# Kernel tuning notes

Hardware: AMD Instinct MI355X
Metric: run time of the kernel (lower is better)

Reference implementation:

```python
import jax, jax.numpy as jnp
import numpy as np

B, T, D = 8, 2048, 1024   # batch, seq_len (== block_size), n_embed
HS = 128                   # head_size

def setup_inputs() -> dict:
    key = jax.random.key(0)
    kx, kk, kq, kv = jax.random.split(key, 4)
    s = D ** -0.5  # torch Linear default init scale ~ U(-1/sqrt(in), 1/sqrt(in))
    x  = jax.random.normal(kx, (B, T, D), dtype=jnp.float32)
    Wk = jax.random.uniform(kk, (HS, D), jnp.float32, -s, s)
    Wq = jax.random.uniform(kq, (HS, D), jnp.float32, -s, s)
    Wv = jax.random.uniform(kv, (HS, D), jnp.float32, -s, s)
    return {"x": x, "Wk": Wk, "Wq": Wq, "Wv": Wv}

def reference(x, Wk, Wq, Wv):
    # single-head causal self-attention; dropout disabled (eval mode)
    Tlen = x.shape[1]
    k = jnp.einsum('btd,hd->bth', x, Wk)   # [B,T,HS]
    q = jnp.einsum('btd,hd->bth', x, Wq)
    v = jnp.einsum('btd,hd->bth', x, Wv)
    scale = Wk.shape[0] ** -0.5
    scores = jnp.einsum('bth,bsh->bts', q, k) * scale   # [B,T,T]
    causal = jnp.tril(jnp.ones((Tlen, Tlen), dtype=bool))
    scores = jnp.where(causal, scores, -jnp.inf)
    weights = jax.nn.softmax(scores, axis=-1)
    out = jnp.einsum('bts,bsh->bth', weights, v)        # [B,T,HS]
    return out
```

## Files before the change

### kernel.cpp

```cpp
#include <hip/hip_runtime.h>
#include <hip/hip_bf16.h>
#include <math.h>

#define BATCH_N 8
#define SEQ_T   2048
#define DIM_D   1024
#define HS_N    128

using bf16x8_t = __attribute__((ext_vector_type(8))) __bf16;
using bf16x4_t = __attribute__((ext_vector_type(4))) __bf16;
using f32x4_t  = __attribute__((ext_vector_type(4))) float;

__device__ __forceinline__ f32x4_t mfma_16x16x32(bf16x8_t a, bf16x8_t b, f32x4_t c) {
  return __builtin_amdgcn_mfma_f32_16x16x32_bf16(a, b, c, 0, 0, 0);
}

__device__ __forceinline__ void async_cp16(const void* g, void* l) {
  __builtin_amdgcn_global_load_lds(
      (const __attribute__((address_space(1))) unsigned int*)g,
      (__attribute__((address_space(3))) unsigned int*)l, 16, 0, 0);
}

#define BAR()      __builtin_amdgcn_s_barrier()
#define FENCE()    asm volatile("" ::: "memory")
#define WAIT_VM(n) asm volatile("s_waitcnt vmcnt(" #n ")" ::: "memory")
#define WAIT_LGKM0 asm volatile("s_waitcnt lgkmcnt(0)" ::: "memory")

__global__ __launch_bounds__(256) void castw_kernel(
    const float* __restrict__ Wk, const float* __restrict__ Wq,
    const float* __restrict__ Wv, __bf16* __restrict__ Wb,
    unsigned int* __restrict__ km) {
  if (blockIdx.x == 0 && threadIdx.x < 8) km[threadIdx.x] = 0u;
  int idx = blockIdx.x * 256 + threadIdx.x;
  int e   = idx * 4;
  int row = e >> 10;
  int col = e & 1023;
  const float* src;
  float sc = 1.0f;
  if (row < 128) {
    src = Wk + row * DIM_D + col;
  } else if (row < 256) {
    src = Wq + (row - 128) * DIM_D + col;
    sc  = 0.08838834764831845f;
  } else {
    src = Wv + (row - 256) * DIM_D + col;
  }
  float4 v = *(const float4*)src;
  bf16x4_t o;
  o[0] = (__bf16)(v.x * sc); o[1] = (__bf16)(v.y * sc);
  o[2] = (__bf16)(v.z * sc); o[3] = (__bf16)(v.w * sc);
  *(bf16x4_t*)(Wb + e) = o;
}

__global__ __launch_bounds__(256, 2) void proj_kernel(
    const float* __restrict__ x, const __bf16* __restrict__ Wb,
    __bf16* __restrict__ Qb, __bf16* __restrict__ Kb, __bf16* __restrict__ Vt,
    unsigned int* __restrict__ km) {
  __shared__ __align__(16) char psmem[57344];

  const int tid  = threadIdx.x;
  const int lane = tid & 63;
  const int wave = tid >> 6;
  const int lr = lane & 15;
  const int lq = lane >> 4;
  const int m0 = blockIdx.x * 32;

  f32x4_t acc[2][6];
  #pragma unroll
  for (int mt = 0; mt < 2; ++mt)
    #pragma unroll
    for (int nt = 0; nt < 6; ++nt) acc[mt][nt] = (f32x4_t){0.f, 0.f, 0.f, 0.f};

  auto stageA = [&](int kt) {
    char* As = psmem + (kt & 1) * 4096;
    const int row = wave * 8 + (lane >> 3);
    const int u16 = lane & 7;
    const int su16 = (((u16 >> 1) ^ (row & 3)) << 1) | (u16 & 1);
    async_cp16(x + (size_t)(m0 + row) * DIM_D + kt * 32 + su16 * 4,
               As + wave * 1024);
  };

  auto stageB = [&](int kt) {
    __bf16* Bs = (__bf16*)(psmem + 8192 + (kt & 1) * 24576);
    for (int c = wave; c < 24; c += 4) {
      const int row = c * 16 + (lane >> 2);
      const int u   = (lane & 3) ^ ((row >> 1) & 3);
      async_cp16(Wb + (size_t)row * DIM_D + kt * 32 + u * 8, Bs + c * 512);
    }
  };

  stageA(0);
  stageB(0);
  __syncthreads();

  for (int kt = 0; kt < 32; ++kt) {
    if (kt + 1 < 32) {
      stageA(kt + 1);
      stageB(kt + 1);
      WAIT_VM(7);
    } else {
      WAIT_VM(0);
    }
    BAR();
    FENCE();

    const float*  As = (const float*)(psmem + (kt & 1) * 4096);
    const __bf16* Bs = (const __bf16*)(psmem + 8192 + (kt & 1) * 24576);

    bf16x8_t af[2];
    #pragma unroll
    for (int mt = 0; mt < 2; ++mt) {
      const int ml   = mt * 16 + lr;
      const int u32r = lq ^ (ml & 3);
      f32x4_t lo = *(const f32x4_t*)(As + ml * 32 + u32r * 8);
      f32x4_t hi = *(const f32x4_t*)(As + ml * 32 + u32r * 8 + 4);
      bf16x8_t a;
      a[0] = (__bf16)lo[0]; a[1] = (__bf16)lo[1];
      a[2] = (__bf16)lo[2]; a[3] = (__bf16)lo[3];
      a[4] = (__bf16)hi[0]; a[5] = (__bf16)hi[1];
      a[6] = (__bf16)hi[2]; a[7] = (__bf16)hi[3];
      af[mt] = a;
    }
    bf16x8_t bfv[6];
    #pragma unroll
    for (int nt = 0; nt < 6; ++nt) {
      const int nl = wave * 96 + nt * 16 + lr;
      bfv[nt] = *(const bf16x8_t*)(&Bs[nl * 32 + ((lq ^ ((nl >> 1) & 3)) * 8)]);
    }
    #pragma unroll
    for (int mt = 0; mt < 2; ++mt)
      #pragma unroll
      for (int nt = 0; nt < 6; ++nt)
        acc[mt][nt] = mfma_16x16x32(af[mt], bfv[nt], acc[mt][nt]);
    WAIT_LGKM0;
    BAR();
    FENCE();
  }

  __syncthreads();
  float* rowss = (float*)psmem;
  if (tid < 32) rowss[tid] = 0.f;
  __syncthreads();
  if (wave < 2) {
    #pragma unroll
    for (int mt = 0; mt < 2; ++mt)
      #pragma unroll
      for (int r = 0; r < 4; ++r) {
        float s = 0.f;
        #pragma unroll
        for (int nt = 0; nt < 6; ++nt)
          if (wave == 0 || nt < 2) s += acc[mt][nt][r] * acc[mt][nt][r];
        s += __shfl_xor(s, 1); s += __shfl_xor(s, 2);
        s += __shfl_xor(s, 4); s += __shfl_xor(s, 8);
        if (lr == 0) atomicAdd(&rowss[mt * 16 + lq * 4 + r], s);
      }
  }
  __syncthreads();
  if (tid < 32) {
    float v = rowss[tid];
    #pragma unroll
    for (int off = 1; off < 32; off <<= 1) v = fmaxf(v, __shfl_xor(v, off));
    if (tid == 0) atomicMax(km + (m0 >> 11), __float_as_uint(v));
  }

  #pragma unroll
  for (int mt = 0; mt < 2; ++mt) {
    const int t0 = m0 + mt * 16 + lq * 4;
    #pragma unroll
    for (int nt = 0; nt < 6; ++nt) {
      const int nn = wave * 96 + nt * 16 + lr;
      if (nn < 256) {
        __bf16* dst = (nn < 128) ? (Kb + nn) : (Qb + (nn - 128));
        #pragma unroll
        for (int r = 0; r < 4; ++r)
          dst[(size_t)(t0 + r) * HS_N] = (__bf16)acc[mt][nt][r];
      } else {
        const int bb = t0 >> 11;
        const int tl = t0 & 2047;
        bf16x4_t o;
        #pragma unroll
        for (int r = 0; r < 4; ++r) o[r] = (__bf16)acc[mt][nt][r];
        *(bf16x4_t*)(Vt + (size_t)bb * (HS_N * SEQ_T) + (size_t)(nn - 256) * SEQ_T + tl) = o;
      }
    }
  }
}

__global__ __launch_bounds__(256, 2) void attn_kernel(
    const __bf16* __restrict__ Qb, const __bf16* __restrict__ Kb,
    const __bf16* __restrict__ Vt, const unsigned int* __restrict__ km,
    __bf16* __restrict__ Opart, float* __restrict__ lpart) {
  __shared__ __align__(16) char smem[81920];
  __bf16* KsBase = (__bf16*)smem;
  __bf16* VsBase = (__bf16*)(smem + 32768);
  float*  Ofl    = (float*)smem;

  const int lane = threadIdx.x & 63;
  const int wave = threadIdx.x >> 6;
  const int lr = lane & 15;
  const int lq = lane >> 4;
  const int bid  = blockIdx.x;
  const int b    = bid & 7;
  const int rest = bid >> 3;
  const int jg   = 15 - (rest >> 2);
  const int p4   = rest & 3;
  const int Q0   = jg * 128;
  const int qa   = Q0 + wave * 32;
  const int ch   = 2 * (jg + 1);
  const int c0   = (p4 * ch) >> 2;
  const int c1   = ((p4 + 1) * ch) >> 2;

  const __bf16* Qbb = Qb + (size_t)b * (SEQ_T * HS_N);
  const __bf16* Kbb = Kb + (size_t)b * (SEQ_T * HS_N);
  const __bf16* Vbb = Vt + (size_t)b * (HS_N * SEQ_T);
  __bf16* pbA = (__bf16*)(smem + 65536 + wave * 4096);
  __bf16* pbB = (__bf16*)(smem + 65536 + wave * 4096 + 2048);

  bf16x8_t qf[2][4];
  #pragma unroll
  for (int t = 0; t < 2; ++t)
    #pragma unroll
    for (int ks = 0; ks < 4; ++ks)
      qf[t][ks] = *(const bf16x8_t*)(Qbb + (size_t)(qa + t * 16 + lr) * HS_N
                                     + ks * 32 + lq * 8);

  const float km2 = __uint_as_float(km[b]);
  float mrow[2][4];
  #pragma unroll
  for (int t = 0; t < 2; ++t) {
    float qn2 = 0.f;
    #pragma unroll
    for (int ks = 0; ks < 4; ++ks)
      #pragma unroll
      for (int j = 0; j < 8; ++j) { float f = (float)qf[t][ks][j]; qn2 += f * f; }
    qn2 += __shfl_xor(qn2, 16);
    qn2 += __shfl_xor(qn2, 32);
    #pragma unroll
    for (int r2 = 0; r2 < 4; ++r2)
      mrow[t][r2] = sqrtf(__shfl(qn2, lq * 4 + r2) * km2);
  }

  f32x4_t Oa[2][8];
  #pragma unroll
  for (int t = 0; t < 2; ++t)
    #pragma unroll
    for (int o = 0; o < 8; ++o) Oa[t][o] = (f32x4_t){0.f, 0.f, 0.f, 0.f};
  float lsum[2][4] = {{0.f,0.f,0.f,0.f},{0.f,0.f,0.f,0.f}};

  auto stage = [&](int bufi, int c) {
    const int kk = c * 64;
    __bf16* Ks = KsBase + bufi * 8192;
    for (int idx = wave; idx < 32; idx += 4) {
      if (idx < 16) {
        const int row = idx * 4 + (lane >> 4);
        const int u   = (lane & 15) ^ (row & 15);
        async_cp16(Kbb + (size_t)(kk + row) * HS_N + u * 8, Ks + idx * 512);
      } else {
        const int i2  = idx - 16;
        const int row = i2 * 8 + (lane >> 3);
        const int u   = (lane & 7) ^ (row & 7);
        async_cp16(Vbb + (size_t)row * SEQ_T + kk + u * 8, VsBase + bufi * 8192 + i2 * 512);
      }
    }
  };

  if (c0 < c1) stage(0, c0);
  __syncthreads();

  for (int c = c0; c < c1; ++c) {
    const int cur = (c - c0) & 1;
    if (c + 1 < c1) {
      stage(cur ^ 1, c + 1);
      WAIT_VM(8);
    } else {
      WAIT_VM(0);
    }
    BAR();
    FENCE();

    const int kk = c * 64;
    const __bf16* Ks = KsBase + cur * 8192;
    const __bf16* Vs = VsBase + cur * 8192;

    f32x4_t s0[4], s1[4];
    #pragma unroll
    for (int nt = 0; nt < 4; ++nt) {
      s0[nt] = (f32x4_t){0.f, 0.f, 0.f, 0.f};
      s1[nt] = (f32x4_t){0.f, 0.f, 0.f, 0.f};
    }
    #pragma unroll
    for (int ks = 0; ks < 4; ++ks)
      #pragma unroll
      for (int nt = 0; nt < 4; ++nt) {
        bf16x8_t kf = *(const bf16x8_t*)(
            &Ks[(nt * 16 + lr) * 128 + (((ks * 4 + lq) ^ lr) * 8)]);
        s0[nt] = mfma_16x16x32(qf[0][ks], kf, s0[nt]);
        s1[nt] = mfma_16x16x32(qf[1][ks], kf, s1[nt]);
      }
    const int q0a = qa, q0b = qa + 16;
    if (kk + 63 > q0a) {
      #pragma unroll
      for (int nt = 0; nt < 4; ++nt) {
        const int col = kk + nt * 16 + lr;
        #pragma unroll
        for (int r2 = 0; r2 < 4; ++r2)
          if (col > q0a + lq * 4 + r2) s0[nt][r2] = -INFINITY;
      }
    }
    if (kk + 63 > q0b) {
      #pragma unroll
      for (int nt = 0; nt < 4; ++nt) {
        const int col = kk + nt * 16 + lr;
        #pragma unroll
        for (int r2 = 0; r2 < 4; ++r2)
          if (col > q0b + lq * 4 + r2) s1[nt][r2] = -INFINITY;
      }
    }

    #pragma unroll
    for (int r2 = 0; r2 < 4; ++r2) {
      float a0 = __expf(s0[0][r2] - mrow[0][r2]);
      float a1 = __expf(s0[1][r2] - mrow[0][r2]);
      float a2 = __expf(s0[2][r2] - mrow[0][r2]);
      float a3 = __expf(s0[3][r2] - mrow[0][r2]);
      s0[0][r2] = a0; s0[1][r2] = a1; s0[2][r2] = a2; s0[3][r2] = a3;
      lsum[0][r2] += (a0 + a1) + (a2 + a3);
      float b0 = __expf(s1[0][r2] - mrow[1][r2]);
      float b1 = __expf(s1[1][r2] - mrow[1][r2]);
      float b2 = __expf(s1[2][r2] - mrow[1][r2]);
      float b3 = __expf(s1[3][r2] - mrow[1][r2]);
      s1[0][r2] = b0; s1[1][r2] = b1; s1[2][r2] = b2; s1[3][r2] = b3;
      lsum[1][r2] += (b0 + b1) + (b2 + b3);
    }

    #pragma unroll
    for (int nt = 0; nt < 4; ++nt)
      #pragma unroll
      for (int r2 = 0; r2 < 4; ++r2) {
        const int prow = lq * 4 + r2;
        const int pcol = (nt * 16 + lr) ^ ((prow & 7) << 3);
        pbA[prow * 64 + pcol] = (__bf16)s0[nt][r2];
        pbB[prow * 64 + pcol] = (__bf16)s1[nt][r2];
      }

    #pragma unroll
    for (int k2 = 0; k2 < 2; ++k2) {
      const int au = ((k2 * 4 + lq) ^ (lr & 7)) << 3;
      bf16x8_t afrA = *(const bf16x8_t*)(pbA + lr * 64 + au);
      bf16x8_t afrB = *(const bf16x8_t*)(pbB + lr * 64 + au);
      #pragma unroll
      for (int o = 0; o < 8; ++o) {
        bf16x8_t vfr = *(const bf16x8_t*)(
            &Vs[(o * 16 + lr) * 64 + (((k2 * 4 + lq) ^ (lr & 7)) * 8)]);
        Oa[0][o] = mfma_16x16x32(afrA, vfr, Oa[0][o]);
        Oa[1][o] = mfma_16x16x32(afrB, vfr, Oa[1][o]);
      }
    }
    WAIT_LGKM0;
    BAR();
    FENCE();
  }

  #pragma unroll
  for (int t = 0; t < 2; ++t)
    #pragma unroll
    for (int r2 = 0; r2 < 4; ++r2) {
      float v = lsum[t][r2];
      v += __shfl_xor(v, 1);
      v += __shfl_xor(v, 2);
      v += __shfl_xor(v, 4);
      v += __shfl_xor(v, 8);
      if (lr == 0)
        lpart[bid * 128 + wave * 32 + t * 16 + lq * 4 + r2] = v;
    }

  #pragma unroll
  for (int t = 0; t < 2; ++t)
    #pragma unroll
    for (int o = 0; o < 8; ++o)
      #pragma unroll
      for (int r2 = 0; r2 < 4; ++r2)
        Ofl[(wave * 32 + t * 16 + lq * 4 + r2) * 132 + o * 16 + lr] = Oa[t][o][r2];
  __syncthreads();

  {
    const int row = threadIdx.x >> 1;
    const int cb  = (threadIdx.x & 1) * 64;
    __bf16* dst = Opart + ((size_t)bid * 128 + row) * 128 + cb;
    #pragma unroll
    for (int g2 = 0; g2 < 16; ++g2) {
      float4 f = *(const float4*)(&Ofl[row * 132 + cb + g2 * 4]);
      bf16x4_t o;
      o[0] = (__bf16)f.x; o[1] = (__bf16)f.y; o[2] = (__bf16)f.z; o[3] = (__bf16)f.w;
      *(bf16x4_t*)(dst + g2 * 4) = o;
    }
  }
}

__global__ __launch_bounds__(256) void merge_kernel(
    const __bf16* __restrict__ Opart, const float* __restrict__ lpart,
    float* __restrict__ out) {
  const int idx = blockIdx.x * 256 + threadIdx.x;
  const int row = idx >> 5;
  const int c4  = (idx & 31) * 4;
  const int b   = row >> 11;
  const int tl  = row & 2047;
  const int jg  = tl >> 7;
  const int lrow = tl & 127;
  const int rbase = (15 - jg) * 4;
  float a0 = 0.f, a1 = 0.f, a2 = 0.f, a3 = 0.f, l = 0.f;
  #pragma unroll
  for (int p = 0; p < 4; ++p) {
    const int s = b + 8 * (rbase + p);
    bf16x4_t a = *(const bf16x4_t*)(Opart + ((size_t)s * 128 + lrow) * 128 + c4);
    a0 += (float)a[0]; a1 += (float)a[1]; a2 += (float)a[2]; a3 += (float)a[3];
    l += lpart[s * 128 + lrow];
  }
  const float inv = 1.0f / l;
  float4 o;
  o.x = a0 * inv; o.y = a1 * inv; o.z = a2 * inv; o.w = a3 * inv;
  *(float4*)(out + (size_t)row * HS_N + c4) = o;
}

extern "C" void kernel_launch(void* const* d_in, const int* in_sizes, int n_in,
                              void* d_out, int out_size, void* d_ws, size_t ws_size,
                              hipStream_t stream) {
  const float* x  = (const float*)d_in[0];
  const float* Wk = (const float*)d_in[1];
  const float* Wq = (const float*)d_in[2];
  const float* Wv = (const float*)d_in[3];
  float* out = (float*)d_out;

  char* ws = (char*)d_ws;
  __bf16* Wb = (__bf16*)ws;
  __bf16* Qb = (__bf16*)(ws + 786432);
  __bf16* Kb = (__bf16*)(ws + 786432 + 4194304);
  __bf16* Vt = (__bf16*)(ws + 786432 + 8388608);
  unsigned int* km = (unsigned int*)(ws + 13369344);
  __bf16* Opart = (__bf16*)(ws + 13369600);
  float*  lpart = (float*)(ws + 30146816);

  castw_kernel<<<384, 256, 0, stream>>>(Wk, Wq, Wv, Wb, km);
  proj_kernel<<<512, 256, 0, stream>>>(x, Wb, Qb, Kb, Vt, km);
  attn_kernel<<<512, 256, 0, stream>>>(Qb, Kb, Vt, km, Opart, lpart);
  merge_kernel<<<2048, 256, 0, stream>>>(Opart, lpart, out);
}
```

Measured before the change: 165.0 us.

## Double projection block rows to 64 with 8 waves sharing weight tiles

The projection kernel now uses 512-thread blocks that each cover 64 token rows instead of 32. Two groups of four waves split the M dimension while sharing the staged weight tile, so each weight tile loaded from global memory serves twice as many rows and the grid halves. The x-tile swizzle changes to an 8-way XOR pattern and the vmcnt wait is adjusted for the new per-thread load count. In exchange, LDS use per block grows to 64KB and there are fewer blocks to spread across CUs.

Measured after the change: 159.1 us. 3.6% less time.

```diff
diff --git a/kernel.cpp b/kernel.cpp
--- a/kernel.cpp
+++ b/kernel.cpp
@@ -52,18 +52,20 @@
   *(bf16x4_t*)(Wb + e) = o;
 }
 
-__global__ __launch_bounds__(256, 2) void proj_kernel(
+__global__ __launch_bounds__(512, 2) void proj_kernel(
     const float* __restrict__ x, const __bf16* __restrict__ Wb,
     __bf16* __restrict__ Qb, __bf16* __restrict__ Kb, __bf16* __restrict__ Vt,
     unsigned int* __restrict__ km) {
-  __shared__ __align__(16) char psmem[57344];
+  __shared__ __align__(16) char psmem[65536];
 
   const int tid  = threadIdx.x;
   const int lane = tid & 63;
   const int wave = tid >> 6;
+  const int h    = wave >> 2;
+  const int g    = wave & 3;
   const int lr = lane & 15;
   const int lq = lane >> 4;
-  const int m0 = blockIdx.x * 32;
+  const int m0 = blockIdx.x * 64;
 
   f32x4_t acc[2][6];
   #pragma unroll
@@ -72,17 +74,17 @@
     for (int nt = 0; nt < 6; ++nt) acc[mt][nt] = (f32x4_t){0.f, 0.f, 0.f, 0.f};
 
   auto stageA = [&](int kt) {
-    char* As = psmem + (kt & 1) * 4096;
-    const int row = wave * 8 + (lane >> 3);
-    const int u16 = lane & 7;
-    const int su16 = (((u16 >> 1) ^ (row & 3)) << 1) | (u16 & 1);
-    async_cp16(x + (size_t)(m0 + row) * DIM_D + kt * 32 + su16 * 4,
+    char* As = psmem + (kt & 1) * 8192;
+    const int r = wave * 8 + (lane >> 3);
+    const int c = (lane & 7) ^ ((lane >> 3) & 7);
+    async_cp16(x + (size_t)(m0 + r) * DIM_D + kt * 32 + c * 4,
                As + wave * 1024);
   };
 
   auto stageB = [&](int kt) {
-    __bf16* Bs = (__bf16*)(psmem + 8192 + (kt & 1) * 24576);
-    for (int c = wave; c < 24; c += 4) {
+    __bf16* Bs = (__bf16*)(psmem + 16384 + (kt & 1) * 24576);
+    #pragma unroll
+    for (int c = wave; c < 24; c += 8) {
       const int row = c * 16 + (lane >> 2);
       const int u   = (lane & 3) ^ ((row >> 1) & 3);
       async_cp16(Wb + (size_t)row * DIM_D + kt * 32 + u * 8, Bs + c * 512);
@@ -91,29 +93,29 @@
 
   stageA(0);
   stageB(0);
-  __syncthreads();
 
   for (int kt = 0; kt < 32; ++kt) {
     if (kt + 1 < 32) {
       stageA(kt + 1);
       stageB(kt + 1);
-      WAIT_VM(7);
+      WAIT_VM(4);
     } else {
       WAIT_VM(0);
     }
     BAR();
     FENCE();
 
-    const float*  As = (const float*)(psmem + (kt & 1) * 4096);
-    const __bf16* Bs = (const __bf16*)(psmem + 8192 + (kt & 1) * 24576);
+    const float*  As = (const float*)(psmem + (kt & 1) * 8192);
+    const __bf16* Bs = (const __bf16*)(psmem + 16384 + (kt & 1) * 24576);
 
     bf16x8_t af[2];
     #pragma unroll
     for (int mt = 0; mt < 2; ++mt) {
-      const int ml   = mt * 16 + lr;
-      const int u32r = lq ^ (ml & 3);
-      f32x4_t lo = *(const f32x4_t*)(As + ml * 32 + u32r * 8);
-      f32x4_t hi = *(const f32x4_t*)(As + ml * 32 + u32r * 8 + 4);
+      const int ml = h * 32 + mt * 16 + lr;
+      const int u0 = (lq * 2)     ^ (ml & 7);
+      const int u1 = (lq * 2 + 1) ^ (ml & 7);
+      f32x4_t lo = *(const f32x4_t*)(As + ml * 32 + u0 * 4);
+      f32x4_t hi = *(const f32x4_t*)(As + ml * 32 + u1 * 4);
       bf16x8_t a;
       a[0] = (__bf16)lo[0]; a[1] = (__bf16)lo[1];
       a[2] = (__bf16)lo[2]; a[3] = (__bf16)lo[3];
@@ -124,7 +126,7 @@
     bf16x8_t bfv[6];
     #pragma unroll
     for (int nt = 0; nt < 6; ++nt) {
-      const int nl = wave * 96 + nt * 16 + lr;
+      const int nl = g * 96 + nt * 16 + lr;
       bfv[nt] = *(const bf16x8_t*)(&Bs[nl * 32 + ((lq ^ ((nl >> 1) & 3)) * 8)]);
     }
     #pragma unroll
@@ -139,9 +141,9 @@
 
   __syncthreads();
   float* rowss = (float*)psmem;
-  if (tid < 32) rowss[tid] = 0.f;
+  if (tid < 64) rowss[tid] = 0.f;
   __syncthreads();
-  if (wave < 2) {
+  if (g < 2) {
     #pragma unroll
     for (int mt = 0; mt < 2; ++mt)
       #pragma unroll
@@ -149,26 +151,26 @@
         float s = 0.f;
         #pragma unroll
         for (int nt = 0; nt < 6; ++nt)
-          if (wave == 0 || nt < 2) s += acc[mt][nt][r] * acc[mt][nt][r];
+          if (g == 0 || nt < 2) s += acc[mt][nt][r] * acc[mt][nt][r];
         s += __shfl_xor(s, 1); s += __shfl_xor(s, 2);
         s += __shfl_xor(s, 4); s += __shfl_xor(s, 8);
-        if (lr == 0) atomicAdd(&rowss[mt * 16 + lq * 4 + r], s);
+        if (lr == 0) atomicAdd(&rowss[h * 32 + mt * 16 + lq * 4 + r], s);
       }
   }
   __syncthreads();
-  if (tid < 32) {
+  if (tid < 64) {
     float v = rowss[tid];
     #pragma unroll
-    for (int off = 1; off < 32; off <<= 1) v = fmaxf(v, __shfl_xor(v, off));
+    for (int off = 1; off < 64; off <<= 1) v = fmaxf(v, __shfl_xor(v, off));
     if (tid == 0) atomicMax(km + (m0 >> 11), __float_as_uint(v));
   }
 
   #pragma unroll
   for (int mt = 0; mt < 2; ++mt) {
-    const int t0 = m0 + mt * 16 + lq * 4;
+    const int t0 = m0 + h * 32 + mt * 16 + lq * 4;
     #pragma unroll
     for (int nt = 0; nt < 6; ++nt) {
-      const int nn = wave * 96 + nt * 16 + lr;
+      const int nn = g * 96 + nt * 16 + lr;
       if (nn < 256) {
         __bf16* dst = (nn < 128) ? (Kb + nn) : (Qb + (nn - 128));
         #pragma unroll
@@ -441,7 +443,7 @@
   float*  lpart = (float*)(ws + 30146816);
 
   castw_kernel<<<384, 256, 0, stream>>>(Wk, Wq, Wv, Wb, km);
-  proj_kernel<<<512, 256, 0, stream>>>(x, Wb, Qb, Kb, Vt, km);
+  proj_kernel<<<256, 512, 0, stream>>>(x, Wb, Qb, Kb, Vt, km);
   attn_kernel<<<512, 256, 0, stream>>>(Qb, Kb, Vt, km, Opart, lpart);
   merge_kernel<<<2048, 256, 0, stream>>>(Opart, lpart, out);
 }
```
